# Kernel tuning notes

Measured on AMD Instinct MI355X. Metric: run time of the kernel, lower is better.

## Reference

```python
import jax, jax.numpy as jnp
import numpy as np
import math

N = 100000; NFEAT = 500; M = 512; HIDDEN = 128; NLAYER = 2; K = 10; NCLASS = 40; ALPHA = 0.1


def setup_inputs() -> dict:
    key = jax.random.key(0)
    ks = jax.random.split(key, 20)
    s_in = 1.0 / math.sqrt(NFEAT); s_h = 1.0 / math.sqrt(HIDDEN); s_e = 1.0 / math.sqrt(HIDDEN + 1)
    kvec = jnp.arange(K + 1, dtype=jnp.float32)
    fW = ALPHA * (1.0 - ALPHA) ** kvec
    fW = fW.at[-1].set((1.0 - ALPHA) ** K)
    return {
        "x": jax.random.normal(ks[0], (N, NFEAT), jnp.float32),
        "e0": jax.random.uniform(ks[1], (M,), jnp.float32) * 2.0,
        "e1": jax.random.uniform(ks[2], (M,), jnp.float32) * 2.0,
        "u0": jax.random.normal(ks[3], (N, M), jnp.float32) / math.sqrt(N),
        "u1": jax.random.normal(ks[4], (N, M), jnp.float32) / math.sqrt(N),
        "fe_w1": jax.random.uniform(ks[5], (NFEAT, HIDDEN), jnp.float32, -s_in, s_in),
        "fe_b1": jnp.zeros((HIDDEN,), jnp.float32),
        "fe_w2": jax.random.uniform(ks[6], (HIDDEN, HIDDEN), jnp.float32, -s_h, s_h),
        "fe_b2": jnp.zeros((HIDDEN,), jnp.float32),
        "eig_w": jax.random.uniform(ks[7], (HIDDEN + 1, 1), jnp.float32, -s_e, s_e),
        "eig_b": jnp.zeros((1,), jnp.float32),
        "layer_weight": 0.01 * jax.random.normal(ks[8], (NLAYER, 2, HIDDEN), jnp.float32),
        "ln_gamma": jnp.ones((NLAYER, HIDDEN), jnp.float32),
        "ln_beta": jnp.zeros((NLAYER, HIDDEN), jnp.float32),
        "fW": fW,
        "att0": jax.random.uniform(ks[9], (HIDDEN, 1), jnp.float32, -1.0, 1.0),
        "att1": jax.random.uniform(ks[10], (HIDDEN, 1), jnp.float32, -1.0, 1.0),
        "att2": jax.random.uniform(ks[11], (HIDDEN, 1), jnp.float32, -1.0, 1.0),
        "att_vec": jax.random.uniform(ks[12], (3, 3), jnp.float32, -1.0 / math.sqrt(3.0), 1.0 / math.sqrt(3.0)),
        "lin3_w": jax.random.uniform(ks[13], (HIDDEN, NCLASS), jnp.float32, -s_h, s_h),
        "lin3_b": jnp.zeros((NCLASS,), jnp.float32),
    }


def _fourier_encode(e, eig_w, eig_b):
    # e: [m] -> [m, 1]; constant-1 column then cos(k*pi*e), k=1..HIDDEN
    freqs = jnp.arange(1, HIDDEN + 1, dtype=e.dtype)
    eeig = jnp.concatenate([jnp.ones((e.shape[0], 1), e.dtype),
                            jnp.cos(math.pi * e[:, None] * freqs)], axis=1)
    return eeig @ eig_w + eig_b  # [m, 1]


def _mfnn_layer(feats, w, g, b):
    # feats: [N, 2, H]; weight [2, H] -> sum over bases, LayerNorm, ReLU
    h = jnp.sum(feats * w, axis=1)
    mu = jnp.mean(h, axis=-1, keepdims=True)
    var = jnp.var(h, axis=-1, keepdims=True)
    h = (h - mu) * jax.lax.rsqrt(var + 1e-5) * g + b
    return jax.nn.relu(h)


def reference(x, e0, e1, u0, u1, fe_w1, fe_b1, fe_w2, fe_b2, eig_w, eig_b,
              layer_weight, ln_gamma, ln_beta, fW, att0, att1, att2, att_vec,
              lin3_w, lin3_b):
    h = jax.nn.relu(x @ fe_w1 + fe_b1) @ fe_w2 + fe_b2  # feat_encoder (dropouts are eval no-ops)
    result = [h]
    tail = jnp.sum(fW[1:])  # r is invariant across the K inner steps: hidden = fW[0]*h + sum(fW[1:])*r
    for e_i, u_i in ((e0, u0), (e1, u1)):
        eig = _fourier_encode(e_i, eig_w, eig_b)  # [m, 1]
        for L in range(NLAYER):
            utx = u_i.T @ h                # [m, H]
            r = u_i @ (eig * utx)          # [N, H] spectral propagation
            hidden = h * fW[0] + tail * r
            feats = jnp.stack([h, hidden], axis=1)  # [N, 2, H]
            h = _mfnn_layer(feats, layer_weight[L], ln_gamma[L], ln_beta[L])
        result.append(h)
    logits = jax.nn.sigmoid(jnp.concatenate(
        [result[0] @ att0, result[1] @ att1, result[2] @ att2], axis=1)) @ att_vec
    att = jax.nn.softmax(logits, axis=1)  # [N, 3]
    h = att[:, 0:1] * result[0] + att[:, 1:2] * result[1] + att[:, 2:3] * result[2]
    return jax.nn.log_softmax(h @ lin3_w + lin3_b, axis=1)
```

## Files before the change

### kernel.cpp

```cpp
#include <hip/hip_runtime.h>
#include <stdint.h>

#define NR 100000L
#define KC 92
#define CHN 1088L

typedef __attribute__((ext_vector_type(8))) short s16x8;
typedef __attribute__((ext_vector_type(4))) short s16x4;
typedef __attribute__((ext_vector_type(4))) float f32x4;

__device__ __forceinline__ unsigned short f2bf(float f) {
  union { float f; unsigned u; } v; v.f = f;
  unsigned r = v.u + 0x7FFFu + ((v.u >> 16) & 1u);
  return (unsigned short)(r >> 16);
}
__device__ __forceinline__ float bf2f(unsigned short s) {
  union { unsigned u; float f; } v; v.u = ((unsigned)s) << 16;
  return v.f;
}
__device__ __forceinline__ f32x4 MF(s16x8 a, s16x8 b, f32x4 c) {
  return __builtin_amdgcn_mfma_f32_16x16x32_bf16(a, b, c, 0, 0, 0);
}


__device__ __forceinline__ int swz(int row, int col) {
  return row * 64 + (((col >> 3) ^ (row & 7)) << 3) + (col & 7);
}

__device__ __forceinline__ void gld16(const void* g, void* l) {
  __builtin_amdgcn_global_load_lds(
      (const __attribute__((address_space(1))) void*)g,
      (__attribute__((address_space(3))) void*)l, 16, 0, 0);
}

template<int ROWS>
__device__ __forceinline__ void stage_async(unsigned short* lds, const unsigned short* src,
    long pitch, long r0, long k0, int tid) {
  const int lane = tid & 63, w = tid >> 6;
  const int lr = lane >> 3, lc = lane & 7;
#pragma unroll
  for (int it = 0; it < ROWS / 32; ++it) {
    const int rowbase = w * (ROWS / 4) + it * 8;
    const int row = rowbase + lr;
    const int sc = lc ^ (row & 7);
    gld16(src + (r0 + row) * pitch + k0 + sc * 8, lds + rowbase * 64);
  }
}

template<int ROWS>
__device__ __forceinline__ void stage_guard(unsigned short* lds, const unsigned short* src,
    long pitch, long r0, long rlim, long k0, long klim, int tid) {
  const int f8 = tid & 7;
#pragma unroll
  for (int it = 0; it < ROWS / 32; ++it) {
    const int row = (tid >> 3) + it * 32;
    const long gr = r0 + row, gk = k0 + f8 * 8;
    s16x8 v = {};
    if (gr < rlim && gk < klim) v = *(const s16x8*)(src + gr * pitch + gk);
    *(s16x8*)(lds + row * 64 + ((f8 ^ (row & 7)) << 3)) = v;
  }
}

template<int ROWS>
__device__ __forceinline__ void stage_guard_f32(unsigned short* lds, const float* src,
    long pitch, long r0, long rlim, long k0, long klim, int tid) {
  const int f4 = tid & 15;
#pragma unroll
  for (int it = 0; it < ROWS / 16; ++it) {
    const int row = (tid >> 4) + it * 16;
    const long gr = r0 + row, gk = k0 + f4 * 4;
    f32x4 v = {};
    if (gr < rlim && gk < klim) v = *(const f32x4*)(src + gr * pitch + gk);
    s16x4 o;
    o[0] = (short)f2bf(v[0]); o[1] = (short)f2bf(v[1]);
    o[2] = (short)f2bf(v[2]); o[3] = (short)f2bf(v[3]);
    const int c = f4 >> 1, h = f4 & 1;
    *(s16x4*)(lds + row * 64 + ((c ^ (row & 7)) << 3) + h * 4) = o;
  }
}

__device__ __forceinline__ void stage_utr_f32(unsigned short* lds, const float* u,
    long n0, long m0, int tid) {
  const int mm = tid & 63;
  const int base = tid >> 6;
#pragma unroll
  for (int it = 0; it < 16; ++it) {
    const int nl = base + it * 4;
    const long n = n0 + nl;
    unsigned short v = 0;
    if (n < NR) v = f2bf(u[n * 512 + m0 + mm]);
    lds[swz(mm, nl)] = v;
  }
}

__device__ __forceinline__ s16x8 fragA(const unsigned short* lds, int row, int kk, int lane) {
  const int c = kk * 4 + (lane >> 4);
  return *(const s16x8*)(lds + row * 64 + ((c ^ (row & 7)) << 3));
}

__global__ void k_prep(const float* __restrict__ e0, const float* __restrict__ e1,
    const float* __restrict__ fe_w1, const float* __restrict__ fe_w2,
    const float* __restrict__ eig_w, const float* __restrict__ eig_b,
    const float* __restrict__ lw, const float* __restrict__ fW,
    unsigned short* __restrict__ W1T, unsigned short* __restrict__ W2T,
    float* __restrict__ eig, float* __restrict__ coef) {
  long id = (long)blockIdx.x * 256 + threadIdx.x;
  if (id < 65536) {
    int j = (int)(id >> 9), k = (int)(id & 511);
    W1T[id] = (k < 500) ? f2bf(fe_w1[(long)k * 128 + j]) : (unsigned short)0;
  } else if (id < 65536 + 16384) {
    long q = id - 65536; int j = (int)(q >> 7), k = (int)(q & 127);
    W2T[q] = f2bf(fe_w2[(long)k * 128 + j]);
  } else if (id < 65536 + 16384 + 1024) {
    long q = id - 65536 - 16384; int b = (int)(q >> 9), m = (int)(q & 511);
    const float* e = b ? e1 : e0;
    float s = eig_b[0] + eig_w[0];
    float pe = 3.14159265358979323846f * e[m];
    for (int f = 1; f <= 128; ++f) s += cosf(pe * (float)f) * eig_w[f];
    eig[q] = s;
  } else if (id < 65536 + 16384 + 1024 + 256) {
    long q = id - 65536 - 16384 - 1024; int L = (int)(q >> 7), j = (int)(q & 127);
    float tail = 0.f;
    for (int k = 1; k <= 10; ++k) tail += fW[k];
    float w0 = lw[L * 256 + j], w1 = lw[L * 256 + 128 + j];
    coef[L * 256 + j] = w0 + fW[0] * w1;
    coef[L * 256 + 128 + j] = tail * w1;
  }
}

__global__ __launch_bounds__(256) void k_cvtx(const float* __restrict__ x,
    unsigned short* __restrict__ xb) {
  const long t = (long)blockIdx.x * 256 + threadIdx.x;
  const int k4 = (int)(t & 127) * 4;
  const long n = t >> 7;
  s16x4 o = {};
  if (k4 < 500) {
    f32x4 v = *(const f32x4*)(x + n * 500 + k4);
    o[0] = (short)f2bf(v[0]); o[1] = (short)f2bf(v[1]);
    o[2] = (short)f2bf(v[2]); o[3] = (short)f2bf(v[3]);
  }
  *(s16x4*)(xb + n * 512 + k4) = o;
}

__global__ __launch_bounds__(256) void k_cvtT(const float* __restrict__ u,
    unsigned short* __restrict__ Ubf, unsigned short* __restrict__ UbT) {
  __shared__ float T[64][68];
  const int tid = threadIdx.x;
  const int nt = blockIdx.x >> 3, mt = blockIdx.x & 7;
  const long n0 = (long)nt * 64, m0 = (long)mt * 64;
  const int c8 = (tid & 7) * 8;
  const int r = tid >> 3;
#pragma unroll
  for (int p = 0; p < 2; ++p) {
    const int rr = r + p * 32;
    const long n = n0 + rr;
    f32x4 a = {}, b = {};
    if (n < NR) {
      a = *(const f32x4*)(u + n * 512 + m0 + c8);
      b = *(const f32x4*)(u + n * 512 + m0 + c8 + 4);
    }
    *(f32x4*)&T[rr][c8] = a;
    *(f32x4*)&T[rr][c8 + 4] = b;
    if (n < NR) {
      s16x8 o;
      o[0] = (short)f2bf(a[0]); o[1] = (short)f2bf(a[1]);
      o[2] = (short)f2bf(a[2]); o[3] = (short)f2bf(a[3]);
      o[4] = (short)f2bf(b[0]); o[5] = (short)f2bf(b[1]);
      o[6] = (short)f2bf(b[2]); o[7] = (short)f2bf(b[3]);
      *(s16x8*)(Ubf + n * 512 + m0 + c8) = o;
    }
  }
  __syncthreads();
  const int nb8 = (tid & 7) * 8;
#pragma unroll
  for (int p = 0; p < 2; ++p) {
    const int mm = r + p * 32;
    s16x8 o;
#pragma unroll
    for (int e = 0; e < 8; ++e) o[e] = (short)f2bf(T[nb8 + e][mm]);
    const long nb = n0 + nb8;
    if (nb + 7 < NR) {
      *(s16x8*)(UbT + (long)(m0 + mm) * NR + nb) = o;
    } else {
#pragma unroll
      for (int e = 0; e < 8; ++e)
        if (nb + e < NR) UbT[(long)(m0 + mm) * NR + nb + e] = o[e];
    }
  }
}

__global__ __launch_bounds__(256) void k_gemm1(const unsigned short* __restrict__ xb,
    const unsigned short* __restrict__ W1T, const float* __restrict__ b1,
    unsigned short* __restrict__ t) {
  __shared__ __align__(16) unsigned short Al[128 * 64];
  __shared__ __align__(16) unsigned short Bl[128 * 64];
  const int tid = threadIdx.x, lane = tid & 63, w = tid >> 6;
  const long n0 = (long)blockIdx.x * 128;
  const bool edge = (n0 + 128) > NR;
  f32x4 acc[2][8] = {};
  for (int kt = 0; kt < 8; ++kt) {
    if (!edge) stage_async<128>(Al, xb, 512, n0, kt * 64L, tid);
    else       stage_guard<128>(Al, xb, 512, n0, NR, kt * 64L, 512, tid);
    stage_async<128>(Bl, W1T, 512, 0, kt * 64L, tid);
    __syncthreads();
#pragma unroll
    for (int kk = 0; kk < 2; ++kk) {
      s16x8 af0 = fragA(Al, w * 32 + (lane & 15), kk, lane);
      s16x8 af1 = fragA(Al, w * 32 + 16 + (lane & 15), kk, lane);
#pragma unroll
      for (int ct = 0; ct < 8; ++ct) {
        s16x8 bfr = fragA(Bl, ct * 16 + (lane & 15), kk, lane);
        acc[0][ct] = MF(af0, bfr, acc[0][ct]);
        acc[1][ct] = MF(af1, bfr, acc[1][ct]);
      }
    }
    __syncthreads();
  }
  const int cl = lane & 15, g = lane >> 4;
#pragma unroll
  for (int ct = 0; ct < 8; ++ct) {
    const int j = ct * 16 + cl;
    const float bias = b1[j];
#pragma unroll
    for (int rt = 0; rt < 2; ++rt)
#pragma unroll
      for (int r = 0; r < 4; ++r) {
        const long n = n0 + w * 32 + rt * 16 + (g << 2) + r;
        if (n < NR) {
          float v = acc[rt][ct][r] + bias;
          t[n * 128 + j] = f2bf(v > 0.f ? v : 0.f);
        }
      }
  }
}

__global__ __launch_bounds__(256) void k_gemm1f(const float* __restrict__ x,
    const unsigned short* __restrict__ W1T, const float* __restrict__ b1,
    unsigned short* __restrict__ t) {
  __shared__ __align__(16) unsigned short Al[64 * 64];
  __shared__ __align__(16) unsigned short Bl[128 * 64];
  const int tid = threadIdx.x, lane = tid & 63, w = tid >> 6;
  const long n0 = (long)blockIdx.x * 64;
  f32x4 acc[8] = {};
  for (int kt = 0; kt < 8; ++kt) {
    stage_guard_f32<64>(Al, x, 500, n0, NR, kt * 64L, 500, tid);
    stage_guard<128>(Bl, W1T, 512, 0, 1L << 40, kt * 64L, 512, tid);
    __syncthreads();
#pragma unroll
    for (int kk = 0; kk < 2; ++kk) {
      s16x8 af = fragA(Al, (w << 4) + (lane & 15), kk, lane);
#pragma unroll
      for (int ct = 0; ct < 8; ++ct) {
        s16x8 bfr = fragA(Bl, (ct << 4) + (lane & 15), kk, lane);
        acc[ct] = MF(af, bfr, acc[ct]);
      }
    }
    __syncthreads();
  }
  const int cl = lane & 15, g = lane >> 4;
#pragma unroll
  for (int ct = 0; ct < 8; ++ct) {
    int j = (ct << 4) + cl;
    float bias = b1[j];
#pragma unroll
    for (int r = 0; r < 4; ++r) {
      long n = n0 + (w << 4) + (g << 2) + r;
      if (n < NR) {
        float v = acc[ct][r] + bias;
        t[n * 128 + j] = f2bf(v > 0.f ? v : 0.f);
      }
    }
  }
}

__global__ __launch_bounds__(256) void k_gemm2(const unsigned short* __restrict__ W2T,
    const unsigned short* __restrict__ t, const float* __restrict__ b2,
    unsigned short* __restrict__ hT) {
  __shared__ __align__(16) unsigned short Al[128 * 64];
  __shared__ __align__(16) unsigned short Bl[128 * 64];
  const int tid = threadIdx.x, lane = tid & 63, w = tid >> 6;
  const long n0 = (long)blockIdx.x * 128;
  const bool edge = (n0 + 128) > NR;
  f32x4 acc[8][2] = {};
  for (int kt = 0; kt < 2; ++kt) {
    stage_async<128>(Al, W2T, 128, 0, kt * 64L, tid);
    if (!edge) stage_async<128>(Bl, t, 128, n0, kt * 64L, tid);
    else       stage_guard<128>(Bl, t, 128, n0, NR, kt * 64L, 128, tid);
    __syncthreads();
#pragma unroll
    for (int kk = 0; kk < 2; ++kk) {
      s16x8 bf0 = fragA(Bl, w * 32 + (lane & 15), kk, lane);
      s16x8 bf1 = fragA(Bl, w * 32 + 16 + (lane & 15), kk, lane);
#pragma unroll
      for (int rt = 0; rt < 8; ++rt) {
        s16x8 af = fragA(Al, rt * 16 + (lane & 15), kk, lane);
        acc[rt][0] = MF(af, bf0, acc[rt][0]);
        acc[rt][1] = MF(af, bf1, acc[rt][1]);
      }
    }
    __syncthreads();
  }
  const int cl = lane & 15, g = lane >> 4;
#pragma unroll
  for (int rt = 0; rt < 8; ++rt)
#pragma unroll
    for (int r = 0; r < 4; ++r) {
      const int j = rt * 16 + (g << 2) + r;
      const float bias = b2[j];
#pragma unroll
      for (int ct = 0; ct < 2; ++ct) {
        const long n = n0 + w * 32 + ct * 16 + cl;
        if (n < NR) hT[(long)j * NR + n] = f2bf(acc[rt][ct][r] + bias);
      }
    }
}

__global__ __launch_bounds__(256) void k_utx(const unsigned short* __restrict__ hT,
    const unsigned short* __restrict__ UbT, float* __restrict__ P) {
  __shared__ __align__(16) unsigned short Al[128 * 64];
  __shared__ __align__(16) unsigned short Bl[128 * 64];
  const int tid = threadIdx.x, lane = tid & 63, w = tid >> 6;
  const int mt = blockIdx.x & 3, c = blockIdx.x >> 2;
  const long m0 = (long)mt * 128, nb = (long)c * CHN;
  f32x4 acc[8][2] = {};
  for (int kt = 0; kt < 17; ++kt) {
    const long n0 = nb + kt * 64;
    if (n0 + 64 <= NR) {
      stage_async<128>(Al, hT, NR, 0, n0, tid);
      stage_async<128>(Bl, UbT, NR, m0, n0, tid);
    } else {
      stage_guard<128>(Al, hT, NR, 0, 1L << 40, n0, NR, tid);
      stage_guard<128>(Bl, UbT, NR, m0, 1L << 40, n0, NR, tid);
    }
    __syncthreads();
#pragma unroll
    for (int kk = 0; kk < 2; ++kk) {
      s16x8 bf0 = fragA(Bl, w * 32 + (lane & 15), kk, lane);
      s16x8 bf1 = fragA(Bl, w * 32 + 16 + (lane & 15), kk, lane);
#pragma unroll
      for (int rt = 0; rt < 8; ++rt) {
        s16x8 af = fragA(Al, rt * 16 + (lane & 15), kk, lane);
        acc[rt][0] = MF(af, bf0, acc[rt][0]);
        acc[rt][1] = MF(af, bf1, acc[rt][1]);
      }
    }
    __syncthreads();
  }
  const int cl = lane & 15, g = lane >> 4;
  float* Pc = P + (long)c * 65536;
#pragma unroll
  for (int rt = 0; rt < 8; ++rt)
#pragma unroll
    for (int r = 0; r < 4; ++r) {
      const int j = rt * 16 + (g << 2) + r;
#pragma unroll
      for (int ct = 0; ct < 2; ++ct) {
        const long m = m0 + w * 32 + ct * 16 + cl;
        Pc[(long)j * 512 + m] = acc[rt][ct][r];
      }
    }
}

__global__ __launch_bounds__(256) void k_utx0(const unsigned short* __restrict__ hT,
    const float* __restrict__ u, float* __restrict__ P) {
  __shared__ __align__(16) unsigned short Al[128 * 64];
  __shared__ __align__(16) unsigned short Bl[64 * 64];
  const int tid = threadIdx.x, lane = tid & 63, w = tid >> 6;
  const int mt = blockIdx.x & 7, c = blockIdx.x >> 3;
  const long m0 = (long)mt * 64, nb = (long)c * CHN;
  f32x4 acc[8] = {};
  for (int kt = 0; kt < 17; ++kt) {
    const long n0 = nb + kt * 64;
    stage_guard<128>(Al, hT, NR, 0, 1L << 40, n0, NR, tid);
    stage_utr_f32(Bl, u, n0, m0, tid);
    __syncthreads();
#pragma unroll
    for (int kk = 0; kk < 2; ++kk) {
      s16x8 bfr = fragA(Bl, (w << 4) + (lane & 15), kk, lane);
#pragma unroll
      for (int rt = 0; rt < 8; ++rt) {
        s16x8 af = fragA(Al, (rt << 4) + (lane & 15), kk, lane);
        acc[rt] = MF(af, bfr, acc[rt]);
      }
    }
    __syncthreads();
  }
  const int cl = lane & 15, g = lane >> 4;
  const long m = m0 + (w << 4) + cl;
  float* Pc = P + (long)c * 65536;
#pragma unroll
  for (int rt = 0; rt < 8; ++rt)
#pragma unroll
    for (int r = 0; r < 4; ++r) {
      int j = (rt << 4) + (g << 2) + r;
      Pc[(long)j * 512 + m] = acc[rt][r];
    }
}

__global__ void k_reduce(const float* __restrict__ P, const float* __restrict__ eig,
                         unsigned short* __restrict__ sT) {
  const int idx = blockIdx.x * 256 + threadIdx.x;
  const int m = idx & 511;
  float s = 0.f;
#pragma unroll 4
  for (int c = 0; c < KC; ++c) s += P[(long)c * 65536 + idx];
  sT[idx] = f2bf(s * eig[m]);
}

__global__ __launch_bounds__(256) void k_rgemm(const unsigned short* __restrict__ sT,
    const unsigned short* __restrict__ Ubf, const unsigned short* __restrict__ hin,
    unsigned short* __restrict__ hout, const float* __restrict__ c0,
    const float* __restrict__ c1, const float* __restrict__ gam,
    const float* __restrict__ bet) {
  __shared__ __align__(16) unsigned short Al[128 * 64];
  __shared__ __align__(16) unsigned short Bl[64 * 64];
  const int tid = threadIdx.x, lane = tid & 63, w = tid >> 6;
  const long n0 = (long)blockIdx.x * 64;
  const bool edge = (n0 + 64) > NR;
  f32x4 acc[8] = {};
  for (int kt = 0; kt < 8; ++kt) {
    stage_async<128>(Al, sT, 512, 0, kt * 64L, tid);
    if (!edge) stage_async<64>(Bl, Ubf, 512, n0, kt * 64L, tid);
    else       stage_guard<64>(Bl, Ubf, 512, n0, NR, kt * 64L, 512, tid);
    __syncthreads();
#pragma unroll
    for (int kk = 0; kk < 2; ++kk) {
      s16x8 bfr = fragA(Bl, (w << 4) + (lane & 15), kk, lane);
#pragma unroll
      for (int rt = 0; rt < 8; ++rt) {
        s16x8 af = fragA(Al, rt * 16 + (lane & 15), kk, lane);
        acc[rt] = MF(af, bfr, acc[rt]);
      }
    }
    __syncthreads();
  }
  if (!edge) stage_async<128>(Al, hin, NR, 0, n0, tid);
  else       stage_guard<128>(Al, hin, NR, 0, 1L << 40, n0, NR, tid);
  __syncthreads();
  const int cl = lane & 15, g = lane >> 4;
  const int nl = (w << 4) + cl;
  float sum = 0.f, ssq = 0.f;
#pragma unroll
  for (int rt = 0; rt < 8; ++rt)
#pragma unroll
    for (int r = 0; r < 4; ++r) {
      const int j = rt * 16 + (g << 2) + r;
      const float hp = bf2f(Al[swz(j, nl)]);
      const float pv = hp * c0[j] + c1[j] * acc[rt][r];
      acc[rt][r] = pv;
      sum += pv; ssq += pv * pv;
    }
  sum += __shfl_xor(sum, 16, 64); sum += __shfl_xor(sum, 32, 64);
  ssq += __shfl_xor(ssq, 16, 64); ssq += __shfl_xor(ssq, 32, 64);
  const float mu = sum * (1.f / 128.f);
  const float rs = rsqrtf(ssq * (1.f / 128.f) - mu * mu + 1e-5f);
  __syncthreads();
#pragma unroll
  for (int rt = 0; rt < 8; ++rt)
#pragma unroll
    for (int r = 0; r < 4; ++r) {
      const int j = rt * 16 + (g << 2) + r;
      float o = (acc[rt][r] - mu) * rs * gam[j] + bet[j];
      Al[swz(j, nl)] = f2bf(o > 0.f ? o : 0.f);
    }
  __syncthreads();
  const int f8 = tid & 7;
  const long gk = n0 + f8 * 8;
#pragma unroll
  for (int it = 0; it < 4; ++it) {
    const int j = (tid >> 3) + it * 32;
    const s16x8 v = *(const s16x8*)(Al + j * 64 + ((f8 ^ (j & 7)) << 3));
    if (gk + 7 < NR) {
      *(s16x8*)(hout + (long)j * NR + gk) = v;
    } else {
#pragma unroll
      for (int e = 0; e < 8; ++e)
        if (gk + e < NR) hout[(long)j * NR + gk + e] = v[e];
    }
  }
}

__global__ __launch_bounds__(256) void k_rgemm64(const unsigned short* __restrict__ sT,
    const float* __restrict__ u, const unsigned short* __restrict__ hin,
    unsigned short* __restrict__ hout, const float* __restrict__ c0,
    const float* __restrict__ c1, const float* __restrict__ gam,
    const float* __restrict__ bet) {
  __shared__ __align__(16) unsigned short Al[128 * 64];
  __shared__ __align__(16) unsigned short Bl[64 * 64];
  const int tid = threadIdx.x, lane = tid & 63, w = tid >> 6;
  const long n0 = (long)blockIdx.x * 64;
  f32x4 acc[8] = {};
  for (int kt = 0; kt < 8; ++kt) {
    stage_guard<128>(Al, sT, 512, 0, 1L << 40, kt * 64L, 512, tid);
    stage_guard_f32<64>(Bl, u, 512, n0, NR, kt * 64L, 512, tid);
    __syncthreads();
#pragma unroll
    for (int kk = 0; kk < 2; ++kk) {
      s16x8 bfr = fragA(Bl, (w << 4) + (lane & 15), kk, lane);
#pragma unroll
      for (int rt = 0; rt < 8; ++rt) {
        s16x8 af = fragA(Al, (rt << 4) + (lane & 15), kk, lane);
        acc[rt] = MF(af, bfr, acc[rt]);
      }
    }
    __syncthreads();
  }
  const int cl = lane & 15, g = lane >> 4;
  const long n = n0 + (w << 4) + cl;
  const bool valid = n < NR;
  float sum = 0.f, ssq = 0.f;
#pragma unroll
  for (int rt = 0; rt < 8; ++rt)
#pragma unroll
    for (int r = 0; r < 4; ++r) {
      int j = (rt << 4) + (g << 2) + r;
      float hp = valid ? bf2f(hin[(long)j * NR + n]) : 0.f;
      float pv = hp * c0[j] + c1[j] * acc[rt][r];
      acc[rt][r] = pv;
      sum += pv; ssq += pv * pv;
    }
  sum += __shfl_xor(sum, 16, 64); sum += __shfl_xor(sum, 32, 64);
  ssq += __shfl_xor(ssq, 16, 64); ssq += __shfl_xor(ssq, 32, 64);
  const float mu = sum * (1.f / 128.f);
  const float rs = rsqrtf(ssq * (1.f / 128.f) - mu * mu + 1e-5f);
  if (valid) {
#pragma unroll
    for (int rt = 0; rt < 8; ++rt)
#pragma unroll
      for (int r = 0; r < 4; ++r) {
        int j = (rt << 4) + (g << 2) + r;
        float o = (acc[rt][r] - mu) * rs * gam[j] + bet[j];
        hout[(long)j * NR + n] = f2bf(o > 0.f ? o : 0.f);
      }
  }
}

__global__ __launch_bounds__(256) void k_final(const unsigned short* __restrict__ R0,
    const unsigned short* __restrict__ R1, const unsigned short* __restrict__ R2,
    const float* __restrict__ att0, const float* __restrict__ att1,
    const float* __restrict__ att2, const float* __restrict__ av,
    const float* __restrict__ W, const float* __restrict__ bias,
    float* __restrict__ out) {
  __shared__ __align__(16) float Wl[128 * 40];
  __shared__ float Av[3][128];
  __shared__ float zb[256 * 41];
  const int tid = threadIdx.x;
  for (int i = tid; i < 5120; i += 256) Wl[i] = W[i];
  if (tid < 128) { Av[0][tid] = att0[tid]; Av[1][tid] = att1[tid]; Av[2][tid] = att2[tid]; }
  __syncthreads();
  const long n0 = (long)blockIdx.x * 256;
  const long n = n0 + tid;
  const long nn = n < NR ? n : NR - 1;
  float a0 = 0.f, a1 = 0.f, a2 = 0.f;
  for (int j = 0; j < 128; ++j) {
    a0 += bf2f(R0[(long)j * NR + nn]) * Av[0][j];
    a1 += bf2f(R1[(long)j * NR + nn]) * Av[1][j];
    a2 += bf2f(R2[(long)j * NR + nn]) * Av[2][j];
  }
  const float s0 = 1.f / (1.f + expf(-a0));
  const float s1 = 1.f / (1.f + expf(-a1));
  const float s2 = 1.f / (1.f + expf(-a2));
  const float l0 = s0 * av[0] + s1 * av[3] + s2 * av[6];
  const float l1 = s0 * av[1] + s1 * av[4] + s2 * av[7];
  const float l2 = s0 * av[2] + s1 * av[5] + s2 * av[8];
  const float mx = fmaxf(l0, fmaxf(l1, l2));
  const float e0v = expf(l0 - mx), e1v = expf(l1 - mx), e2v = expf(l2 - mx);
  const float inv = 1.f / (e0v + e1v + e2v);
  const float w0 = e0v * inv, w1 = e1v * inv, w2 = e2v * inv;
  float z[40];
#pragma unroll
  for (int c = 0; c < 40; ++c) z[c] = bias[c];
  for (int j = 0; j < 128; ++j) {
    const float h = w0 * bf2f(R0[(long)j * NR + nn]) + w1 * bf2f(R1[(long)j * NR + nn])
                  + w2 * bf2f(R2[(long)j * NR + nn]);
#pragma unroll
    for (int c4 = 0; c4 < 10; ++c4) {
      f32x4 wv = *(const f32x4*)(&Wl[j * 40 + c4 * 4]);
      z[c4 * 4 + 0] += h * wv[0];
      z[c4 * 4 + 1] += h * wv[1];
      z[c4 * 4 + 2] += h * wv[2];
      z[c4 * 4 + 3] += h * wv[3];
    }
  }
  float mz = z[0];
#pragma unroll
  for (int c = 1; c < 40; ++c) mz = fmaxf(mz, z[c]);
  float se = 0.f;
#pragma unroll
  for (int c = 0; c < 40; ++c) se += expf(z[c] - mz);
  const float ls = logf(se);
#pragma unroll
  for (int c = 0; c < 40; ++c) zb[tid * 41 + c] = z[c] - mz - ls;
  __syncthreads();
  long rows = NR - n0; if (rows > 256) rows = 256;
  const long cnt = rows * 40;
  for (long i = tid; i < cnt; i += 256)
    out[n0 * 40 + i] = zb[(i / 40) * 41 + (i % 40)];
}

extern "C" void kernel_launch(void* const* d_in, const int* in_sizes, int n_in,
                              void* d_out, int out_size, void* d_ws, size_t ws_size,
                              hipStream_t stream) {
  const float* x      = (const float*)d_in[0];
  const float* e0     = (const float*)d_in[1];
  const float* e1     = (const float*)d_in[2];
  const float* u0     = (const float*)d_in[3];
  const float* u1     = (const float*)d_in[4];
  const float* fe_w1  = (const float*)d_in[5];
  const float* fe_b1  = (const float*)d_in[6];
  const float* fe_w2  = (const float*)d_in[7];
  const float* fe_b2  = (const float*)d_in[8];
  const float* eig_w  = (const float*)d_in[9];
  const float* eig_bi = (const float*)d_in[10];
  const float* lw     = (const float*)d_in[11];
  const float* ln_g   = (const float*)d_in[12];
  const float* ln_b   = (const float*)d_in[13];
  const float* fW     = (const float*)d_in[14];
  const float* att0   = (const float*)d_in[15];
  const float* att1   = (const float*)d_in[16];
  const float* att2   = (const float*)d_in[17];
  const float* attv   = (const float*)d_in[18];
  const float* lin3w  = (const float*)d_in[19];
  const float* lin3b  = (const float*)d_in[20];
  float* out = (float*)d_out;

  const size_t SZ_H = (size_t)NR * 128 * 2;
  const size_t SZ_P = (size_t)KC * 65536 * 4;
  const size_t SZ_U = (size_t)NR * 512 * 2;
  const size_t SZ_X = (size_t)NR * 512 * 2;

  char* p = (char*)d_ws;
  unsigned short* R0T = (unsigned short*)p; p += SZ_H;
  unsigned short* R1T = (unsigned short*)p; p += SZ_H;
  unsigned short* R2T = (unsigned short*)p; p += SZ_H;
  float* P            = (float*)p;          p += SZ_P;
  unsigned short* W1T = (unsigned short*)p; p += 131072;
  unsigned short* W2T = (unsigned short*)p; p += 32768;
  unsigned short* sT  = (unsigned short*)p; p += 131072;
  float* eig          = (float*)p;          p += 4096;
  float* coef         = (float*)p;          p += 2048;
  const size_t base = (size_t)(p - (char*)d_ws);
  const bool full = ws_size >= base + SZ_X + 2 * SZ_U;
  unsigned short* xb  = nullptr;
  unsigned short* UbT = nullptr;
  unsigned short* Ubf = nullptr;
  if (full) {
    xb  = (unsigned short*)p; p += SZ_X;
    UbT = (unsigned short*)p; p += SZ_U;
    Ubf = (unsigned short*)p; p += SZ_U;
  }

  k_prep<<<325, 256, 0, stream>>>(e0, e1, fe_w1, fe_w2, eig_w, eig_bi, lw, fW,
                                  W1T, W2T, eig, coef);
  const int GB64  = (int)((NR + 63) / 64);
  const int GB128 = (int)((NR + 127) / 128);

  if (full) {
    k_cvtx<<<50000, 256, 0, stream>>>(x, xb);
    k_gemm1<<<GB128, 256, 0, stream>>>(xb, W1T, fe_b1, R1T);
  } else {
    k_gemm1f<<<GB64, 256, 0, stream>>>(x, W1T, fe_b1, R1T);
  }
  k_gemm2<<<GB128, 256, 0, stream>>>(W2T, R1T, fe_b2, R0T);

  for (int b = 0; b < 2; ++b) {
    const float* u = b ? u1 : u0;
    if (full) k_cvtT<<<GB64 * 8, 256, 0, stream>>>(u, Ubf, UbT);
    const unsigned short* hin = (b == 0) ? R0T : R1T;
    unsigned short* hb = b ? R2T : R1T;
    for (int L = 0; L < 2; ++L) {
      unsigned short* hout = hb;
      if (full) k_utx<<<4 * KC, 256, 0, stream>>>(hin, UbT, P);
      else      k_utx0<<<8 * KC, 256, 0, stream>>>(hin, u, P);
      k_reduce<<<256, 256, 0, stream>>>(P, eig + b * 512, sT);
      if (full)
        k_rgemm<<<GB64, 256, 0, stream>>>(sT, Ubf, hin, hout,
            coef + L * 256, coef + L * 256 + 128, ln_g + L * 128, ln_b + L * 128);
      else
        k_rgemm64<<<GB64, 256, 0, stream>>>(sT, u, hin, hout,
            coef + L * 256, coef + L * 256 + 128, ln_g + L * 128, ln_b + L * 128);
      hin = hout;
    }
  }
  k_final<<<(int)((NR + 255) / 256), 256, 0, stream>>>(R0T, R1T, R2T,
      att0, att1, att2, attv, lin3w, lin3b, out);
}
```

Measured before the change: 728.3 us.

## Store split-K partials in bf16, vectorize reduce, swizzle transpose LDS tile

Split-K partial sums from the U^T·h kernels are now written as bf16 instead of fp32, which halves partial-buffer traffic, and the reduction kernel reads four bf16 values per thread with fewer blocks. The transpose-convert kernel replaces its padded LDS tile with an XOR-swizzled layout to avoid bank conflicts. k_utx also gets an occupancy hint in its launch bounds. Rounding every partial to bf16 before summing over 92 chunks loses accuracy in the spectral projection.

```diff
diff --git a/kernel.cpp b/kernel.cpp
--- a/kernel.cpp
+++ b/kernel.cpp
@@ -21,7 +21,6 @@
 __device__ __forceinline__ f32x4 MF(s16x8 a, s16x8 b, f32x4 c) {
   return __builtin_amdgcn_mfma_f32_16x16x32_bf16(a, b, c, 0, 0, 0);
 }
-
 
 __device__ __forceinline__ int swz(int row, int col) {
   return row * 64 + (((col >> 3) ^ (row & 7)) << 3) + (col & 7);
@@ -144,12 +143,13 @@
 
 __global__ __launch_bounds__(256) void k_cvtT(const float* __restrict__ u,
     unsigned short* __restrict__ Ubf, unsigned short* __restrict__ UbT) {
-  __shared__ float T[64][68];
+  __shared__ float T[64 * 64];
   const int tid = threadIdx.x;
   const int nt = blockIdx.x >> 3, mt = blockIdx.x & 7;
   const long n0 = (long)nt * 64, m0 = (long)mt * 64;
+  const int r = tid >> 3;
   const int c8 = (tid & 7) * 8;
-  const int r = tid >> 3;
+  const int u0 = c8 >> 2;
 #pragma unroll
   for (int p = 0; p < 2; ++p) {
     const int rr = r + p * 32;
@@ -159,8 +159,9 @@
       a = *(const f32x4*)(u + n * 512 + m0 + c8);
       b = *(const f32x4*)(u + n * 512 + m0 + c8 + 4);
     }
-    *(f32x4*)&T[rr][c8] = a;
-    *(f32x4*)&T[rr][c8 + 4] = b;
+    const int sw = (rr >> 3) & 7;
+    *(f32x4*)&T[rr * 64 + ((u0 ^ sw) << 2)] = a;
+    *(f32x4*)&T[rr * 64 + (((u0 + 1) ^ sw) << 2)] = b;
     if (n < NR) {
       s16x8 o;
       o[0] = (short)f2bf(a[0]); o[1] = (short)f2bf(a[1]);
@@ -172,12 +173,15 @@
   }
   __syncthreads();
   const int nb8 = (tid & 7) * 8;
+  const int sw2 = tid & 7;
 #pragma unroll
   for (int p = 0; p < 2; ++p) {
     const int mm = r + p * 32;
+    const int mu = mm >> 2, ml = mm & 3;
     s16x8 o;
 #pragma unroll
-    for (int e = 0; e < 8; ++e) o[e] = (short)f2bf(T[nb8 + e][mm]);
+    for (int e = 0; e < 8; ++e)
+      o[e] = (short)f2bf(T[(nb8 + e) * 64 + (((mu) ^ sw2) << 2) + ml]);
     const long nb = n0 + nb8;
     if (nb + 7 < NR) {
       *(s16x8*)(UbT + (long)(m0 + mm) * NR + nb) = o;
@@ -315,8 +319,8 @@
     }
 }
 
-__global__ __launch_bounds__(256) void k_utx(const unsigned short* __restrict__ hT,
-    const unsigned short* __restrict__ UbT, float* __restrict__ P) {
+__global__ __launch_bounds__(256, 3) void k_utx(const unsigned short* __restrict__ hT,
+    const unsigned short* __restrict__ UbT, unsigned short* __restrict__ P) {
   __shared__ __align__(16) unsigned short Al[128 * 64];
   __shared__ __align__(16) unsigned short Bl[128 * 64];
   const int tid = threadIdx.x, lane = tid & 63, w = tid >> 6;
@@ -347,7 +351,7 @@
     __syncthreads();
   }
   const int cl = lane & 15, g = lane >> 4;
-  float* Pc = P + (long)c * 65536;
+  unsigned short* Pc = P + (long)c * 65536;
 #pragma unroll
   for (int rt = 0; rt < 8; ++rt)
 #pragma unroll
@@ -356,13 +360,13 @@
 #pragma unroll
       for (int ct = 0; ct < 2; ++ct) {
         const long m = m0 + w * 32 + ct * 16 + cl;
-        Pc[(long)j * 512 + m] = acc[rt][ct][r];
+        Pc[(long)j * 512 + m] = f2bf(acc[rt][ct][r]);
       }
     }
 }
 
 __global__ __launch_bounds__(256) void k_utx0(const unsigned short* __restrict__ hT,
-    const float* __restrict__ u, float* __restrict__ P) {
+    const float* __restrict__ u, unsigned short* __restrict__ P) {
   __shared__ __align__(16) unsigned short Al[128 * 64];
   __shared__ __align__(16) unsigned short Bl[64 * 64];
   const int tid = threadIdx.x, lane = tid & 63, w = tid >> 6;
@@ -387,24 +391,33 @@
   }
   const int cl = lane & 15, g = lane >> 4;
   const long m = m0 + (w << 4) + cl;
-  float* Pc = P + (long)c * 65536;
+  unsigned short* Pc = P + (long)c * 65536;
 #pragma unroll
   for (int rt = 0; rt < 8; ++rt)
 #pragma unroll
     for (int r = 0; r < 4; ++r) {
       int j = (rt << 4) + (g << 2) + r;
-      Pc[(long)j * 512 + m] = acc[rt][r];
-    }
-}
-
-__global__ void k_reduce(const float* __restrict__ P, const float* __restrict__ eig,
+      Pc[(long)j * 512 + m] = f2bf(acc[rt][r]);
+    }
+}
+
+__global__ void k_reduce(const unsigned short* __restrict__ P, const float* __restrict__ eig,
                          unsigned short* __restrict__ sT) {
-  const int idx = blockIdx.x * 256 + threadIdx.x;
+  const int t4 = blockIdx.x * 256 + threadIdx.x;
+  const int idx = t4 * 4;
   const int m = idx & 511;
-  float s = 0.f;
+  float s0 = 0.f, s1 = 0.f, s2 = 0.f, s3 = 0.f;
+  const unsigned short* p = P + idx;
 #pragma unroll 4
-  for (int c = 0; c < KC; ++c) s += P[(long)c * 65536 + idx];
-  sT[idx] = f2bf(s * eig[m]);
+  for (int c = 0; c < KC; ++c) {
+    s16x4 v = *(const s16x4*)(p + (long)c * 65536);
+    s0 += bf2f((unsigned short)v[0]); s1 += bf2f((unsigned short)v[1]);
+    s2 += bf2f((unsigned short)v[2]); s3 += bf2f((unsigned short)v[3]);
+  }
+  s16x4 o;
+  o[0] = (short)f2bf(s0 * eig[m]);     o[1] = (short)f2bf(s1 * eig[m + 1]);
+  o[2] = (short)f2bf(s2 * eig[m + 2]); o[3] = (short)f2bf(s3 * eig[m + 3]);
+  *(s16x4*)(sT + idx) = o;
 }
 
 __global__ __launch_bounds__(256) void k_rgemm(const unsigned short* __restrict__ sT,
@@ -625,7 +638,7 @@
   float* out = (float*)d_out;
 
   const size_t SZ_H = (size_t)NR * 128 * 2;
-  const size_t SZ_P = (size_t)KC * 65536 * 4;
+  const size_t SZ_P = (size_t)KC * 65536 * 2;
   const size_t SZ_U = (size_t)NR * 512 * 2;
   const size_t SZ_X = (size_t)NR * 512 * 2;
 
@@ -633,7 +646,7 @@
   unsigned short* R0T = (unsigned short*)p; p += SZ_H;
   unsigned short* R1T = (unsigned short*)p; p += SZ_H;
   unsigned short* R2T = (unsigned short*)p; p += SZ_H;
-  float* P            = (float*)p;          p += SZ_P;
+  unsigned short* P   = (unsigned short*)p; p += SZ_P;
   unsigned short* W1T = (unsigned short*)p; p += 131072;
   unsigned short* W2T = (unsigned short*)p; p += 32768;
   unsigned short* sT  = (unsigned short*)p; p += 131072;
@@ -672,7 +685,7 @@
       unsigned short* hout = hb;
       if (full) k_utx<<<4 * KC, 256, 0, stream>>>(hin, UbT, P);
       else      k_utx0<<<8 * KC, 256, 0, stream>>>(hin, u, P);
-      k_reduce<<<256, 256, 0, stream>>>(P, eig + b * 512, sT);
+      k_reduce<<<64, 256, 0, stream>>>(P, eig + b * 512, sT);
       if (full)
         k_rgemm<<<GB64, 256, 0, stream>>>(sT, Ubf, hin, hout,
             coef + L * 256, coef + L * 256 + 128, ln_g + L * 128, ln_b + L * 128);
```

Result: no change. 717.1 us (-1.5%).
